# Optimization experiments

Hardware: AMD Instinct MI355X
Metric: run time of the kernel (lower is better)

Reference implementation:

```python
import jax, jax.numpy as jnp
from jax import lax
import numpy as np

B, T, H, OUT = 8, 1500, 1280, 4096
MAXTOK = 375
N_INNER = 3  # 1 mandatory integrate-and-fire iteration + 2 gated extras (alpha<1 => 1 suffices)


def _forward_cif(hidden, alphas, num_tokens, max_tok):
    # hidden: [B, T, D], alphas: [B, T], num_tokens: [B] int32
    Bv, Tv, _ = hidden.shape
    nm1 = num_tokens - 1
    bidx = jnp.arange(Bv)

    def step(carry, xs):
        integrate, token_index = carry  # [B] float, [B] int32
        alpha_t, not_last = xs
        col = jnp.zeros((Bv, max_tok), alphas.dtype)
        alpha = alpha_t
        alpha_needed = 1.0 - integrate
        integrate = integrate + alpha
        ready = integrate >= 1.0
        remainds = jnp.zeros_like(alpha)
        active = jnp.any(ready) | True  # first body iteration always runs (do-while)
        active = jnp.asarray(True)
        for _ in range(N_INNER):
            n_int = jnp.where(ready, integrate - 1.0, integrate)
            a_int = jnp.where(ready, alpha_needed, alpha)
            n_col = col.at[bidx, token_index].set(a_int)
            n_rem = alpha - a_int
            n_tok = jnp.minimum(token_index + ready.astype(token_index.dtype), nm1)
            n_ready = n_int >= 1.0
            integrate = jnp.where(active, n_int, integrate)
            col = jnp.where(active, n_col, col)
            remainds = jnp.where(active, n_rem, remainds)
            token_index = jnp.where(active, n_tok, token_index)
            alpha = jnp.where(active, n_rem, alpha)
            alpha_needed = jnp.where(active, jnp.ones_like(alpha_needed), alpha_needed)
            ready = jnp.where(active, n_ready, jnp.zeros_like(ready))
            active = active & jnp.any(ready)
        # torch adds remainds into column t at step t+1 (so last column never gets it)
        col = jnp.where(not_last, col.at[bidx, token_index].add(remainds), col)
        return (integrate, token_index), col

    init = (jnp.zeros((Bv,), alphas.dtype), jnp.zeros((Bv,), jnp.int32))
    xs = (alphas.T, jnp.arange(Tv) < Tv - 1)  # per-step alpha column, not-last flag
    _, cols = lax.scan(step, init, xs)  # cols: [T, B, max_tok]
    weights = jnp.transpose(cols, (1, 2, 0))  # [B, max_tok, T]
    return jnp.einsum('bmt,btd->bmd', weights, hidden)


def setup_inputs() -> dict:
    key = jax.random.key(0)
    ks = jax.random.split(key, 4)
    audio_features = jax.random.normal(ks[0], (B, T, H), jnp.float32)
    num_tokens = jax.random.randint(ks[1], (B,), 100, MAXTOK + 1).astype(jnp.int32)
    rms_w = jnp.ones((H,), jnp.float32) * 0.4
    cif_w = jax.random.normal(ks[2], (H - 1, H), jnp.float32) / np.sqrt(H - 1)
    cif_b = jnp.zeros((H,), jnp.float32)
    text_w = jax.random.normal(ks[3], (H, OUT), jnp.float32) / np.sqrt(H)
    text_b = jnp.zeros((OUT,), jnp.float32)
    return dict(audio_features=audio_features, num_tokens=num_tokens, rms_w=rms_w,
                cif_w=cif_w, cif_b=cif_b, text_w=text_w, text_b=text_b, max_tokens=MAXTOK)


def reference(audio_features, num_tokens, rms_w, cif_w, cif_b, text_w, text_b, max_tokens):
    alphas = jax.nn.sigmoid(audio_features[:, :, -1])  # [B, T]
    pred_num_tokens = alphas.sum(-1)  # [B]
    alphas = alphas * (num_tokens.astype(alphas.dtype) / pred_num_tokens)[:, None]
    h = _forward_cif(audio_features[:, :, :-1], alphas, num_tokens, max_tokens)  # [B, M, H-1]
    h = h @ cif_w + cif_b  # cif_proj -> [B, M, H]
    d = h.shape[-1]
    rms = jnp.sqrt(jnp.sum(h * h, axis=-1, keepdims=True) / d + 1e-6)
    h = h / rms * rms_w  # RMSNorm(post_ln)
    h = h @ text_w + text_b  # text_proj -> [B, M, OUT]
    return h, pred_num_tokens
```

## Files before the change

kernel.cpp:

```cpp
#include <hip/hip_runtime.h>
#include <hip/hip_bf16.h>
#include <stdint.h>

#define B_ 8
#define T_ 1500
#define H_ 1280
#define HM1 1279
#define OUT_ 4096
#define MTOK 375
#define MROWS (B_*MTOK)
#define KPAD 1280

typedef __attribute__((ext_vector_type(8))) short bf16x8;
typedef __attribute__((ext_vector_type(4))) float f32x4;

static __device__ __forceinline__ unsigned short f2bf(float f) {
    unsigned int x = __float_as_uint(f);
    unsigned int r = (x + 0x7fffu + ((x >> 16) & 1u)) >> 16;
    return (unsigned short)r;
}
static __device__ __forceinline__ float bf2f(unsigned short u) {
    return __uint_as_float(((unsigned int)u) << 16);
}
static __device__ __forceinline__ void glds16(const unsigned short* g, unsigned short* l) {
    __builtin_amdgcn_global_load_lds(
        (const __attribute__((address_space(1))) void*)g,
        (__attribute__((address_space(3))) void*)l, 16, 0, 0);
}

__global__ __launch_bounds__(256) void k_front(
    const float* __restrict__ audio, const int* __restrict__ num_tokens,
    float* __restrict__ pred_out,
    int* __restrict__ tok0, float* __restrict__ w0a,
    int* __restrict__ tok1, float* __restrict__ w1a,
    int* __restrict__ lo, int* __restrict__ hi,
    const float* __restrict__ cif_w, const float* __restrict__ text_w,
    unsigned short* __restrict__ cwt, unsigned short* __restrict__ twt)
{
    __shared__ float smem[3514];
    const int tid = threadIdx.x;

    if (blockIdx.x < B_) {
        const int b = blockIdx.x;
        float* al = smem;
        float* ip = smem + 1500;
        float* red = smem + 3000;
        int*   redI = (int*)(smem + 3256);
        float* scale_sh = smem + 3512;

        float sig[6];
        float s = 0.f;
        #pragma unroll
        for (int i = 0; i < 6; ++i) {
            int t = tid + i*256;
            sig[i] = 0.f;
            if (t < T_) {
                float x = audio[((size_t)b*T_ + t)*H_ + (H_-1)];
                sig[i] = 1.f / (1.f + expf(-x));
                s += sig[i];
            }
        }
        red[tid] = s; __syncthreads();
        for (int off = 128; off > 0; off >>= 1) {
            if (tid < off) red[tid] += red[tid+off];
            __syncthreads();
        }
        if (tid == 0) {
            float pred = red[0];
            pred_out[b] = pred;
            *scale_sh = (float)num_tokens[b] / pred;
        }
        __syncthreads();
        float scale = *scale_sh;
        #pragma unroll
        for (int i = 0; i < 6; ++i) {
            int t = tid + i*256;
            if (t < T_) al[t] = sig[i] * scale;
        }
        for (int m = tid; m < MTOK; m += 256) {
            lo[b*MTOK+m] = T_; hi[b*MTOK+m] = 0;
        }
        if (tid == 0) lo[b*MTOK] = 0;
        __syncthreads();

        if (tid == 0) {
            float integ = 0.f;
            float4 cur = *(const float4*)&al[0];
            for (int t = 0; t < T_; t += 4) {
                float4 nxt = (t + 4 < T_) ? *(const float4*)&al[t+4]
                                          : make_float4(0.f,0.f,0.f,0.f);
                float av[4] = {cur.x, cur.y, cur.z, cur.w};
                float ipv[4];
                #pragma unroll
                for (int j = 0; j < 4; ++j) {
                    ipv[j] = integ;
                    float sx = integ + av[j];
                    integ = (sx >= 1.f) ? (sx - 1.f) : sx;
                }
                *(float4*)&ip[t] = *(float4*)ipv;
                cur = nxt;
            }
        }
        __syncthreads();

        const int t0 = tid * 6;
        const int nm1 = num_tokens[b] - 1;
        int fires[6];
        int cnt = 0;
        if (t0 < T_) {
            #pragma unroll
            for (int j = 0; j < 6; ++j) {
                int t = t0 + j;
                float sx = ip[t] + al[t];
                fires[j] = (sx >= 1.f) ? 1 : 0;
                cnt += fires[j];
            }
        }
        redI[tid] = cnt; __syncthreads();
        #pragma unroll
        for (int off = 1; off < 256; off <<= 1) {
            int v = redI[tid];
            if (tid >= off) v += redI[tid - off];
            __syncthreads();
            redI[tid] = v;
            __syncthreads();
        }
        if (t0 < T_) {
            int F = redI[tid] - cnt;
            const int base = b*T_;
            #pragma unroll
            for (int j = 0; j < 6; ++j) {
                int t = t0 + j;
                float a = al[t], ipv = ip[t];
                int fire = fires[j];
                F += fire;
                int tk1 = min(F, nm1);
                int tk0 = min(F - fire, nm1);
                float w0 = fire ? (1.f - ipv) : a;
                float w1 = (t < T_-1) ? (a - w0) : 0.f;
                tok0[base+t] = tk0;  w0a[base+t] = w0;
                tok1[base+t] = tk1;  w1a[base+t] = w1;
                if (tk1 != tk0) {
                    hi[b*MTOK + tk0] = t + 1;
                    lo[b*MTOK + tk1] = t;
                }
                if (t == T_-1) hi[b*MTOK + tk1] = T_;
            }
        }
    } else {
        float (*tile)[33] = (float(*)[33])smem;
        int blk = blockIdx.x - B_;
        const float* src; unsigned short* dst; int R, C, bx, by;
        if (blk < 1600) { src = cif_w;  dst = cwt; R = HM1; C = H_;   bx = blk % 40;  by = blk / 40; }
        else { blk -= 1600; src = text_w; dst = twt; R = H_;  C = OUT_; bx = blk % 128; by = blk / 128; }
        int c0 = bx * 32, r0 = by * 32;
        int lx = tid & 31, ly = tid >> 5;
        #pragma unroll
        for (int j = 0; j < 4; ++j) {
            int r = r0 + ly + j*8;
            tile[ly + j*8][lx] = (r < R) ? src[(size_t)r*C + c0 + lx] : 0.f;
        }
        __syncthreads();
        #pragma unroll
        for (int j = 0; j < 4; ++j) {
            int c = c0 + ly + j*8;
            dst[(size_t)c*KPAD + r0 + lx] = f2bf(tile[lx][ly + j*8]);
        }
    }
}

__global__ __launch_bounds__(256) void k3_pool(
    const float* __restrict__ audio,
    const int* __restrict__ tok0, const float* __restrict__ w0a,
    const int* __restrict__ tok1, const float* __restrict__ w1a,
    const int* __restrict__ lo, const int* __restrict__ hi,
    unsigned short* __restrict__ h1b)
{
    int bm = blockIdx.x;
    int b = bm / MTOK, m = bm % MTOK;
    int l = lo[bm], h = hi[bm];
    int tid = threadIdx.x;
    float acc[5] = {0.f,0.f,0.f,0.f,0.f};
    for (int t = l; t < h; ++t) {
        int i0 = b*T_ + t;
        float w = 0.f;
        if (tok0[i0] == m) w += w0a[i0];
        if (tok1[i0] == m) w += w1a[i0];
        if (w != 0.f) {
            const float* row = audio + (size_t)i0 * H_;
            #pragma unroll
            for (int i = 0; i < 5; ++i) {
                int d = tid + i*256;
                if (d < HM1) acc[i] += w * row[d];
            }
        }
    }
    unsigned short* dst = h1b + (size_t)bm * KPAD;
    #pragma unroll
    for (int i = 0; i < 5; ++i) {
        int d = tid + i*256;
        dst[d] = (d < HM1) ? f2bf(acc[i]) : (unsigned short)0;
    }
}

template<int TM, bool BF16_OUT>
__global__ __launch_bounds__(256) void mfma_gemm_bt(
    const unsigned short* __restrict__ A, const unsigned short* __restrict__ Bt,
    const float* __restrict__ bias, void* __restrict__ Cv, int M, int N)
{
    constexpr int K = KPAD;
    constexpr int RA = TM / 32;
    constexpr int MI = 4;
    constexpr int NI = (TM == 128) ? 4 : 2;
    __shared__ unsigned short sA[TM*64];
    __shared__ unsigned short sB[128*64];
    const int tid = threadIdx.x;
    const int m0 = blockIdx.y * TM, n0 = blockIdx.x * 128;
    const int wave = tid >> 6, lane = tid & 63;
    const int wm = (TM == 128) ? (wave & 1) * 64 : 0;
    const int wn = (TM == 128) ? (wave >> 1) * 64 : wave * 32;
    const int lrow = lane & 15, quad = lane >> 4;

    const int sr = tid >> 3;
    const int g  = (tid & 7) ^ (sr & 7);
    const unsigned short* Ag[RA];
    #pragma unroll
    for (int p = 0; p < RA; ++p)
        Ag[p] = A + (size_t)min(m0 + sr + 32*p, M - 1) * K + g*8;
    const unsigned short* Bg[4];
    #pragma unroll
    for (int p = 0; p < 4; ++p)
        Bg[p] = Bt + (size_t)(n0 + sr + 32*p) * K + g*8;

    int offA[MI], offB[NI];
    #pragma unroll
    for (int i = 0; i < MI; ++i)
        offA[i] = (wm + i*16 + lrow)*64 + ((quad ^ (lrow & 7)) * 8);
    #pragma unroll
    for (int i = 0; i < NI; ++i)
        offB[i] = (wn + i*16 + lrow)*64 + ((quad ^ (lrow & 7)) * 8);

    f32x4 acc[MI][NI] = {};

    for (int k0 = 0; k0 < K; k0 += 64) {
        #pragma unroll
        for (int p = 0; p < RA; ++p) glds16(Ag[p] + k0, sA + (tid + 256*p)*8);
        #pragma unroll
        for (int p = 0; p < 4;  ++p) glds16(Bg[p] + k0, sB + (tid + 256*p)*8);
        __syncthreads();
        #pragma unroll
        for (int h = 0; h < 2; ++h) {
            const int hx = h * 32;
            bf16x8 af[MI], bfr[NI];
            #pragma unroll
            for (int i = 0; i < MI; ++i) af[i]  = *(const bf16x8*)&sA[offA[i] ^ hx];
            #pragma unroll
            for (int i = 0; i < NI; ++i) bfr[i] = *(const bf16x8*)&sB[offB[i] ^ hx];
            #pragma unroll
            for (int mi = 0; mi < MI; ++mi)
                #pragma unroll
                for (int ni = 0; ni < NI; ++ni)
                    acc[mi][ni] = __builtin_amdgcn_mfma_f32_16x16x32_bf16(
                        af[mi], bfr[ni], acc[mi][ni], 0, 0, 0);
        }
        __syncthreads();
    }

    #pragma unroll
    for (int ni = 0; ni < NI; ++ni) {
        int col = n0 + wn + ni*16 + lrow;
        float bv = bias[col];
        #pragma unroll
        for (int mi = 0; mi < MI; ++mi) {
            int rowb = m0 + wm + mi*16 + quad*4;
            #pragma unroll
            for (int r = 0; r < 4; ++r) {
                int row = rowb + r;
                if (row < M) {
                    float v = acc[mi][ni][r] + bv;
                    if (BF16_OUT) ((unsigned short*)Cv)[(size_t)row*N + col] = f2bf(v);
                    else          ((float*)Cv)[(size_t)row*N + col] = v;
                }
            }
        }
    }
}

__global__ __launch_bounds__(256) void k5_rms_bf16(
    unsigned short* __restrict__ hX, const float* __restrict__ rms_w)
{
    int row = blockIdx.x;
    unsigned short* p = hX + (size_t)row * H_;
    int tid = threadIdx.x;
    float v[5];
    float s = 0.f;
    #pragma unroll
    for (int i = 0; i < 5; ++i) {
        v[i] = bf2f(p[tid + i*256]);
        s += v[i] * v[i];
    }
    __shared__ float red[256];
    red[tid] = s; __syncthreads();
    for (int off = 128; off > 0; off >>= 1) {
        if (tid < off) red[tid] += red[tid+off];
        __syncthreads();
    }
    float inv = 1.f / sqrtf(red[0] / (float)H_ + 1e-6f);
    #pragma unroll
    for (int i = 0; i < 5; ++i) {
        int d = tid + i*256;
        p[d] = f2bf(v[i] * inv * rms_w[d]);
    }
}

extern "C" void kernel_launch(void* const* d_in, const int* in_sizes, int n_in,
                              void* d_out, int out_size, void* d_ws, size_t ws_size,
                              hipStream_t stream) {
    (void)in_sizes; (void)n_in; (void)out_size; (void)ws_size;
    const float* audio      = (const float*)d_in[0];
    const int*   num_tokens = (const int*)d_in[1];
    const float* rms_w      = (const float*)d_in[2];
    const float* cif_w      = (const float*)d_in[3];
    const float* cif_b      = (const float*)d_in[4];
    const float* text_w     = (const float*)d_in[5];
    const float* text_b     = (const float*)d_in[6];

    float* out  = (float*)d_out;
    float* pred = out + (size_t)MROWS * OUT_;

    char* ws = (char*)d_ws;
    float* w0a    = (float*)(ws + 48000);
    float* w1a    = (float*)(ws + 96000);
    int*   tok0   = (int*)  (ws + 144000);
    int*   tok1   = (int*)  (ws + 192000);
    int*   lo     = (int*)  (ws + 240000);
    int*   hi     = (int*)  (ws + 252000);
    unsigned short* h1b = (unsigned short*)(ws + 264192);
    unsigned short* cwt = (unsigned short*)(ws + 7944192);
    unsigned short* twt = (unsigned short*)(ws + 11220992);
    unsigned short* hX  = (unsigned short*)(ws + 21706752);

    k_front<<<B_ + 1600 + 5120, 256, 0, stream>>>(
        audio, num_tokens, pred, tok0, w0a, tok1, w1a, lo, hi,
        cif_w, text_w, cwt, twt);
    k3_pool<<<MROWS, 256, 0, stream>>>(audio, tok0, w0a, tok1, w1a, lo, hi, h1b);
    mfma_gemm_bt<64, true><<<dim3(H_/128, (MROWS+63)/64), 256, 0, stream>>>(
        h1b, cwt, cif_b, hX, MROWS, H_);
    k5_rms_bf16<<<MROWS, 256, 0, stream>>>(hX, rms_w);
    mfma_gemm_bt<128, false><<<dim3(OUT_/128, (MROWS+127)/128), 256, 0, stream>>>(
        hX, twt, text_b, out, MROWS, OUT_);
}
```

Before: 288.9 us.

## Fuse all stages into one persistent cooperative kernel with grid syncs

Replaces the five separate launches (front/transpose, pooling, cif GEMM, RMSNorm, text GEMM) with a single cooperative kernel of 512 blocks that loops over work items and uses grid.sync between stages. The GEMM tile is also changed to a K-step of 32 with a new LDS swizzle so that shared memory fits in 16KB and two blocks can reside per CU. The aim is to remove launch gaps and inter-kernel drain. In exchange it fixes the grid at 512 blocks, which limits parallelism for the many-block stages. The cif GEMM runs on only 470 blocks, and halving the K-step doubles the barriers per tile.

```diff
diff --git a/kernel.cpp b/kernel.cpp
--- a/kernel.cpp
+++ b/kernel.cpp
@@ -1,6 +1,9 @@
 #include <hip/hip_runtime.h>
+#include <hip/hip_cooperative_groups.h>
 #include <hip/hip_bf16.h>
 #include <stdint.h>
+
+namespace cg = cooperative_groups;
 
 #define B_ 8
 #define T_ 1500
@@ -10,38 +13,127 @@
 #define MTOK 375
 #define MROWS (B_*MTOK)
 #define KPAD 1280
+#define GRID_ 512
 
 typedef __attribute__((ext_vector_type(8))) short bf16x8;
 typedef __attribute__((ext_vector_type(4))) float f32x4;
-
-static __device__ __forceinline__ unsigned short f2bf(float f) {
+typedef unsigned short u16;
+
+static __device__ __forceinline__ u16 f2bf(float f) {
     unsigned int x = __float_as_uint(f);
     unsigned int r = (x + 0x7fffu + ((x >> 16) & 1u)) >> 16;
-    return (unsigned short)r;
-}
-static __device__ __forceinline__ float bf2f(unsigned short u) {
+    return (u16)r;
+}
+static __device__ __forceinline__ float bf2f(u16 u) {
     return __uint_as_float(((unsigned int)u) << 16);
 }
-static __device__ __forceinline__ void glds16(const unsigned short* g, unsigned short* l) {
+static __device__ __forceinline__ void glds16(const u16* g, u16* l) {
     __builtin_amdgcn_global_load_lds(
         (const __attribute__((address_space(1))) void*)g,
         (__attribute__((address_space(3))) void*)l, 16, 0, 0);
 }
 
-__global__ __launch_bounds__(256) void k_front(
+template<int TM, bool BF16_OUT>
+static __device__ __forceinline__ void gemm_tile(
+    const u16* __restrict__ A, const u16* __restrict__ Bt,
+    const float* __restrict__ bias, void* __restrict__ Cv,
+    int M, int N, int m0, int n0, u16* sA, u16* sB, int tid)
+{
+    constexpr int K = KPAD;
+    constexpr int RA = TM / 64;
+    constexpr int MI = 4;
+    constexpr int NI = (TM == 128) ? 4 : 2;
+    const int wave = tid >> 6, lane = tid & 63;
+    const int wm = (TM == 128) ? (wave & 1) * 64 : 0;
+    const int wn = (TM == 128) ? (wave >> 1) * 64 : wave * 32;
+    const int lrow = lane & 15, quad = lane >> 4;
+
+    const int r0 = tid >> 2, sl = tid & 3;
+    const int q0 = sl ^ (r0 & 3) ^ ((r0 >> 2) & 3);
+    const u16* Ag[RA];
+    #pragma unroll
+    for (int p = 0; p < RA; ++p)
+        Ag[p] = A + (size_t)min(m0 + r0 + 64*p, M - 1) * K + q0 * 8;
+    const u16* Bg[2];
+    #pragma unroll
+    for (int p = 0; p < 2; ++p)
+        Bg[p] = Bt + (size_t)(n0 + r0 + 64*p) * K + q0 * 8;
+
+    int offA[MI], offB[NI];
+    #pragma unroll
+    for (int i = 0; i < MI; ++i) {
+        int m = wm + i*16 + lrow;
+        offA[i] = m*32 + (quad ^ (m & 3) ^ ((m >> 2) & 3)) * 8;
+    }
+    #pragma unroll
+    for (int i = 0; i < NI; ++i) {
+        int n = wn + i*16 + lrow;
+        offB[i] = n*32 + (quad ^ (n & 3) ^ ((n >> 2) & 3)) * 8;
+    }
+
+    f32x4 acc[MI][NI] = {};
+
+    for (int k0 = 0; k0 < K; k0 += 32) {
+        #pragma unroll
+        for (int p = 0; p < RA; ++p) glds16(Ag[p] + k0, sA + (tid + 256*p)*8);
+        #pragma unroll
+        for (int p = 0; p < 2;  ++p) glds16(Bg[p] + k0, sB + (tid + 256*p)*8);
+        __syncthreads();
+        bf16x8 af[MI], bfr[NI];
+        #pragma unroll
+        for (int i = 0; i < MI; ++i) af[i]  = *(const bf16x8*)&sA[offA[i]];
+        #pragma unroll
+        for (int i = 0; i < NI; ++i) bfr[i] = *(const bf16x8*)&sB[offB[i]];
+        #pragma unroll
+        for (int mi = 0; mi < MI; ++mi)
+            #pragma unroll
+            for (int ni = 0; ni < NI; ++ni)
+                acc[mi][ni] = __builtin_amdgcn_mfma_f32_16x16x32_bf16(
+                    af[mi], bfr[ni], acc[mi][ni], 0, 0, 0);
+        __syncthreads();
+    }
+
+    #pragma unroll
+    for (int ni = 0; ni < NI; ++ni) {
+        int col = n0 + wn + ni*16 + lrow;
+        float bv = bias[col];
+        #pragma unroll
+        for (int mi = 0; mi < MI; ++mi) {
+            int rowb = m0 + wm + mi*16 + quad*4;
+            #pragma unroll
+            for (int r = 0; r < 4; ++r) {
+                int row = rowb + r;
+                if (row < M) {
+                    float v = acc[mi][ni][r] + bv;
+                    if (BF16_OUT) ((u16*)Cv)[(size_t)row*N + col] = f2bf(v);
+                    else          ((float*)Cv)[(size_t)row*N + col] = v;
+                }
+            }
+        }
+    }
+}
+
+__global__ __launch_bounds__(256, 2) void k_mega(
     const float* __restrict__ audio, const int* __restrict__ num_tokens,
-    float* __restrict__ pred_out,
+    const float* __restrict__ rms_w,
+    const float* __restrict__ cif_w, const float* __restrict__ cif_b,
+    const float* __restrict__ text_w, const float* __restrict__ text_b,
+    float* __restrict__ out, float* __restrict__ pred_out,
     int* __restrict__ tok0, float* __restrict__ w0a,
     int* __restrict__ tok1, float* __restrict__ w1a,
     int* __restrict__ lo, int* __restrict__ hi,
-    const float* __restrict__ cif_w, const float* __restrict__ text_w,
-    unsigned short* __restrict__ cwt, unsigned short* __restrict__ twt)
+    u16* __restrict__ h1b, u16* __restrict__ cwt, u16* __restrict__ twt,
+    u16* __restrict__ hX)
 {
-    __shared__ float smem[3514];
+    cg::grid_group grid = cg::this_grid();
+    __shared__ __align__(16) char smem_raw[16384];
     const int tid = threadIdx.x;
-
-    if (blockIdx.x < B_) {
-        const int b = blockIdx.x;
+    const int bid = blockIdx.x;
+    const int G = GRID_;
+
+    if (bid < B_) {
+        const int b = bid;
+        float* smem = (float*)smem_raw;
         float* al = smem;
         float* ip = smem + 1500;
         float* red = smem + 3000;
@@ -148,168 +240,97 @@
             }
         }
     } else {
-        float (*tile)[33] = (float(*)[33])smem;
-        int blk = blockIdx.x - B_;
-        const float* src; unsigned short* dst; int R, C, bx, by;
-        if (blk < 1600) { src = cif_w;  dst = cwt; R = HM1; C = H_;   bx = blk % 40;  by = blk / 40; }
-        else { blk -= 1600; src = text_w; dst = twt; R = H_;  C = OUT_; bx = blk % 128; by = blk / 128; }
-        int c0 = bx * 32, r0 = by * 32;
-        int lx = tid & 31, ly = tid >> 5;
-        #pragma unroll
-        for (int j = 0; j < 4; ++j) {
-            int r = r0 + ly + j*8;
-            tile[ly + j*8][lx] = (r < R) ? src[(size_t)r*C + c0 + lx] : 0.f;
-        }
-        __syncthreads();
-        #pragma unroll
-        for (int j = 0; j < 4; ++j) {
-            int c = c0 + ly + j*8;
-            dst[(size_t)c*KPAD + r0 + lx] = f2bf(tile[lx][ly + j*8]);
-        }
-    }
-}
-
-__global__ __launch_bounds__(256) void k3_pool(
-    const float* __restrict__ audio,
-    const int* __restrict__ tok0, const float* __restrict__ w0a,
-    const int* __restrict__ tok1, const float* __restrict__ w1a,
-    const int* __restrict__ lo, const int* __restrict__ hi,
-    unsigned short* __restrict__ h1b)
-{
-    int bm = blockIdx.x;
-    int b = bm / MTOK, m = bm % MTOK;
-    int l = lo[bm], h = hi[bm];
-    int tid = threadIdx.x;
-    float acc[5] = {0.f,0.f,0.f,0.f,0.f};
-    for (int t = l; t < h; ++t) {
-        int i0 = b*T_ + t;
-        float w = 0.f;
-        if (tok0[i0] == m) w += w0a[i0];
-        if (tok1[i0] == m) w += w1a[i0];
-        if (w != 0.f) {
-            const float* row = audio + (size_t)i0 * H_;
+        float (*tile)[33] = (float(*)[33])smem_raw;
+        for (int idx = bid - B_; idx < 6720; idx += G - B_) {
+            int blk = idx;
+            const float* src; u16* dst; int R, C, bx, by;
+            if (blk < 1600) { src = cif_w;  dst = cwt; R = HM1; C = H_;   bx = blk % 40;  by = blk / 40; }
+            else { blk -= 1600; src = text_w; dst = twt; R = H_;  C = OUT_; bx = blk % 128; by = blk / 128; }
+            int c0 = bx * 32, r0 = by * 32;
+            int lx = tid & 31, ly = tid >> 5;
+            #pragma unroll
+            for (int j = 0; j < 4; ++j) {
+                int r = r0 + ly + j*8;
+                tile[ly + j*8][lx] = (r < R) ? src[(size_t)r*C + c0 + lx] : 0.f;
+            }
+            __syncthreads();
+            #pragma unroll
+            for (int j = 0; j < 4; ++j) {
+                int c = c0 + ly + j*8;
+                dst[(size_t)c*KPAD + r0 + lx] = f2bf(tile[lx][ly + j*8]);
+            }
+            __syncthreads();
+        }
+    }
+    grid.sync();
+
+    for (int bm = bid; bm < MROWS; bm += G) {
+        int b = bm / MTOK, m = bm % MTOK;
+        int l = lo[bm], h = hi[bm];
+        float acc[5] = {0.f,0.f,0.f,0.f,0.f};
+        for (int t = l; t < h; ++t) {
+            int i0 = b*T_ + t;
+            float w = 0.f;
+            if (tok0[i0] == m) w += w0a[i0];
+            if (tok1[i0] == m) w += w1a[i0];
+            if (w != 0.f) {
+                const float* row = audio + (size_t)i0 * H_;
+                #pragma unroll
+                for (int i = 0; i < 5; ++i) {
+                    int d = tid + i*256;
+                    if (d < HM1) acc[i] += w * row[d];
+                }
+            }
+        }
+        u16* dst = h1b + (size_t)bm * KPAD;
+        #pragma unroll
+        for (int i = 0; i < 5; ++i) {
+            int d = tid + i*256;
+            dst[d] = (d < HM1) ? f2bf(acc[i]) : (u16)0;
+        }
+    }
+    grid.sync();
+
+    if (bid < 470) {
+        int by = bid / 10, bx = bid % 10;
+        gemm_tile<64, true>(h1b, cwt, cif_b, hX, MROWS, H_,
+                            by*64, bx*128,
+                            (u16*)smem_raw, (u16*)(smem_raw + 4096), tid);
+    }
+    grid.sync();
+
+    {
+        float* red = (float*)smem_raw;
+        for (int row = bid; row < MROWS; row += G) {
+            u16* p = hX + (size_t)row * H_;
+            float v[5];
+            float s = 0.f;
+            #pragma unroll
+            for (int i = 0; i < 5; ++i) {
+                v[i] = bf2f(p[tid + i*256]);
+                s += v[i] * v[i];
+            }
+            red[tid] = s; __syncthreads();
+            for (int off = 128; off > 0; off >>= 1) {
+                if (tid < off) red[tid] += red[tid+off];
+                __syncthreads();
+            }
+            float inv = 1.f / sqrtf(red[0] / (float)H_ + 1e-6f);
             #pragma unroll
             for (int i = 0; i < 5; ++i) {
                 int d = tid + i*256;
-                if (d < HM1) acc[i] += w * row[d];
-            }
-        }
-    }
-    unsigned short* dst = h1b + (size_t)bm * KPAD;
-    #pragma unroll
-    for (int i = 0; i < 5; ++i) {
-        int d = tid + i*256;
-        dst[d] = (d < HM1) ? f2bf(acc[i]) : (unsigned short)0;
-    }
-}
-
-template<int TM, bool BF16_OUT>
-__global__ __launch_bounds__(256) void mfma_gemm_bt(
-    const unsigned short* __restrict__ A, const unsigned short* __restrict__ Bt,
-    const float* __restrict__ bias, void* __restrict__ Cv, int M, int N)
-{
-    constexpr int K = KPAD;
-    constexpr int RA = TM / 32;
-    constexpr int MI = 4;
-    constexpr int NI = (TM == 128) ? 4 : 2;
-    __shared__ unsigned short sA[TM*64];
-    __shared__ unsigned short sB[128*64];
-    const int tid = threadIdx.x;
-    const int m0 = blockIdx.y * TM, n0 = blockIdx.x * 128;
-    const int wave = tid >> 6, lane = tid & 63;
-    const int wm = (TM == 128) ? (wave & 1) * 64 : 0;
-    const int wn = (TM == 128) ? (wave >> 1) * 64 : wave * 32;
-    const int lrow = lane & 15, quad = lane >> 4;
-
-    const int sr = tid >> 3;
-    const int g  = (tid & 7) ^ (sr & 7);
-    const unsigned short* Ag[RA];
-    #pragma unroll
-    for (int p = 0; p < RA; ++p)
-        Ag[p] = A + (size_t)min(m0 + sr + 32*p, M - 1) * K + g*8;
-    const unsigned short* Bg[4];
-    #pragma unroll
-    for (int p = 0; p < 4; ++p)
-        Bg[p] = Bt + (size_t)(n0 + sr + 32*p) * K + g*8;
-
-    int offA[MI], offB[NI];
-    #pragma unroll
-    for (int i = 0; i < MI; ++i)
-        offA[i] = (wm + i*16 + lrow)*64 + ((quad ^ (lrow & 7)) * 8);
-    #pragma unroll
-    for (int i = 0; i < NI; ++i)
-        offB[i] = (wn + i*16 + lrow)*64 + ((quad ^ (lrow & 7)) * 8);
-
-    f32x4 acc[MI][NI] = {};
-
-    for (int k0 = 0; k0 < K; k0 += 64) {
-        #pragma unroll
-        for (int p = 0; p < RA; ++p) glds16(Ag[p] + k0, sA + (tid + 256*p)*8);
-        #pragma unroll
-        for (int p = 0; p < 4;  ++p) glds16(Bg[p] + k0, sB + (tid + 256*p)*8);
-        __syncthreads();
-        #pragma unroll
-        for (int h = 0; h < 2; ++h) {
-            const int hx = h * 32;
-            bf16x8 af[MI], bfr[NI];
-            #pragma unroll
-            for (int i = 0; i < MI; ++i) af[i]  = *(const bf16x8*)&sA[offA[i] ^ hx];
-            #pragma unroll
-            for (int i = 0; i < NI; ++i) bfr[i] = *(const bf16x8*)&sB[offB[i] ^ hx];
-            #pragma unroll
-            for (int mi = 0; mi < MI; ++mi)
-                #pragma unroll
-                for (int ni = 0; ni < NI; ++ni)
-                    acc[mi][ni] = __builtin_amdgcn_mfma_f32_16x16x32_bf16(
-                        af[mi], bfr[ni], acc[mi][ni], 0, 0, 0);
-        }
-        __syncthreads();
-    }
-
-    #pragma unroll
-    for (int ni = 0; ni < NI; ++ni) {
-        int col = n0 + wn + ni*16 + lrow;
-        float bv = bias[col];
-        #pragma unroll
-        for (int mi = 0; mi < MI; ++mi) {
-            int rowb = m0 + wm + mi*16 + quad*4;
-            #pragma unroll
-            for (int r = 0; r < 4; ++r) {
-                int row = rowb + r;
-                if (row < M) {
-                    float v = acc[mi][ni][r] + bv;
-                    if (BF16_OUT) ((unsigned short*)Cv)[(size_t)row*N + col] = f2bf(v);
-                    else          ((float*)Cv)[(size_t)row*N + col] = v;
-                }
-            }
-        }
-    }
-}
-
-__global__ __launch_bounds__(256) void k5_rms_bf16(
-    unsigned short* __restrict__ hX, const float* __restrict__ rms_w)
-{
-    int row = blockIdx.x;
-    unsigned short* p = hX + (size_t)row * H_;
-    int tid = threadIdx.x;
-    float v[5];
-    float s = 0.f;
-    #pragma unroll
-    for (int i = 0; i < 5; ++i) {
-        v[i] = bf2f(p[tid + i*256]);
-        s += v[i] * v[i];
-    }
-    __shared__ float red[256];
-    red[tid] = s; __syncthreads();
-    for (int off = 128; off > 0; off >>= 1) {
-        if (tid < off) red[tid] += red[tid+off];
-        __syncthreads();
-    }
-    float inv = 1.f / sqrtf(red[0] / (float)H_ + 1e-6f);
-    #pragma unroll
-    for (int i = 0; i < 5; ++i) {
-        int d = tid + i*256;
-        p[d] = f2bf(v[i] * inv * rms_w[d]);
+                p[d] = f2bf(v[i] * inv * rms_w[d]);
+            }
+            __syncthreads();
+        }
+    }
+    grid.sync();
+
+    for (int tile = bid; tile < 32*24; tile += G) {
+        int bx = tile & 31, by = tile >> 5;
+        gemm_tile<128, false>(hX, twt, text_b, out, MROWS, OUT_,
+                              by*128, bx*128,
+                              (u16*)smem_raw, (u16*)(smem_raw + 8192), tid);
     }
 }
 
@@ -329,24 +350,25 @@
     float* pred = out + (size_t)MROWS * OUT_;
 
     char* ws = (char*)d_ws;
-    float* w0a    = (float*)(ws + 48000);
-    float* w1a    = (float*)(ws + 96000);
-    int*   tok0   = (int*)  (ws + 144000);
-    int*   tok1   = (int*)  (ws + 192000);
-    int*   lo     = (int*)  (ws + 240000);
-    int*   hi     = (int*)  (ws + 252000);
-    unsigned short* h1b = (unsigned short*)(ws + 264192);
-    unsigned short* cwt = (unsigned short*)(ws + 7944192);
-    unsigned short* twt = (unsigned short*)(ws + 11220992);
-    unsigned short* hX  = (unsigned short*)(ws + 21706752);
-
-    k_front<<<B_ + 1600 + 5120, 256, 0, stream>>>(
-        audio, num_tokens, pred, tok0, w0a, tok1, w1a, lo, hi,
-        cif_w, text_w, cwt, twt);
-    k3_pool<<<MROWS, 256, 0, stream>>>(audio, tok0, w0a, tok1, w1a, lo, hi, h1b);
-    mfma_gemm_bt<64, true><<<dim3(H_/128, (MROWS+63)/64), 256, 0, stream>>>(
-        h1b, cwt, cif_b, hX, MROWS, H_);
-    k5_rms_bf16<<<MROWS, 256, 0, stream>>>(hX, rms_w);
-    mfma_gemm_bt<128, false><<<dim3(OUT_/128, (MROWS+127)/128), 256, 0, stream>>>(
-        hX, twt, text_b, out, MROWS, OUT_);
-}
+    float* w0a  = (float*)(ws + 48000);
+    float* w1a  = (float*)(ws + 96000);
+    int*   tok0 = (int*)  (ws + 144000);
+    int*   tok1 = (int*)  (ws + 192000);
+    int*   lo   = (int*)  (ws + 240000);
+    int*   hi   = (int*)  (ws + 252000);
+    u16* h1b = (u16*)(ws + 264192);
+    u16* cwt = (u16*)(ws + 7944192);
+    u16* twt = (u16*)(ws + 11220992);
+    u16* hX  = (u16*)(ws + 21706752);
+
+    void* args[] = {
+        (void*)&audio, (void*)&num_tokens, (void*)&rms_w,
+        (void*)&cif_w, (void*)&cif_b, (void*)&text_w, (void*)&text_b,
+        (void*)&out, (void*)&pred,
+        (void*)&tok0, (void*)&w0a, (void*)&tok1, (void*)&w1a,
+        (void*)&lo, (void*)&hi,
+        (void*)&h1b, (void*)&cwt, (void*)&twt, (void*)&hX
+    };
+    hipLaunchCooperativeKernel((const void*)k_mega, dim3(GRID_), dim3(256),
+                               args, 0, stream);
+}
```

Result: slower. 629.2 us (+117.8%).
